# Performance work log

Measured on AMD Instinct MI355X. Metric: run time of the kernel, lower is better.

## Reference

```python
import jax, jax.numpy as jnp
import numpy as np

B, H, P, D = 32, 8, 16, 32
OUT_DIM = 32
GROUPS = 64
NUM_F = 8
N = H * P * D                 # 4096 (self.num)
PHO = P * H * OUT_DIM         # 4096


def setup_inputs() -> dict:
    key = jax.random.key(0)
    ks = jax.random.split(key, 10)
    return {
        "q": jax.random.normal(ks[0], (B, H, P, D), dtype=jnp.float32),
        "k": jax.random.normal(ks[1], (B, H, P, D), dtype=jnp.float32),
        "grid": jnp.arange(NUM_F, dtype=jnp.float32) + 1.0,
        "base_weight_q": jax.random.uniform(ks[2], (PHO, N), dtype=jnp.float32),
        "base_weight_k": jax.random.uniform(ks[3], (PHO, N), dtype=jnp.float32),
        "coef_q": jax.random.uniform(ks[4], (GROUPS, 1, NUM_F), dtype=jnp.float32),
        "coef_k": jax.random.uniform(ks[5], (GROUPS, 1, NUM_F), dtype=jnp.float32),
        # grouped 1x1 conv == num_f independent [PHO, N] matmuls (only conv_layer_q is used in forward)
        "conv_wq": jax.random.normal(ks[6], (NUM_F, PHO, N), dtype=jnp.float32) * 0.01,
        "conv_bq": jax.random.normal(ks[7], (NUM_F, PHO), dtype=jnp.float32) * 0.01,
        "scale_sp": jnp.ones((PHO,), dtype=jnp.float32),
    }


def reference(q, k, grid, base_weight_q, base_weight_k, coef_q, coef_k, conv_wq, conv_bq, scale_sp):
    b, h, p, d = q.shape
    n = h * p * d
    nf = grid.shape[0]
    gs = n // coef_q.shape[0]               # group_size
    out_dim = base_weight_q.shape[0] // (p * h)

    qf = q.reshape(b, n)
    kf = k.reshape(b, n)

    base_q = jax.nn.silu(qf) @ base_weight_q.T          # [B, PHO]
    base_k = jax.nn.silu(kf) @ base_weight_k.T

    # per-feature coef: feature i in group i//gs, scaled per frequency f -> [F, N]
    ce_q = jnp.repeat(coef_q[:, 0, :], gs, axis=0).T
    ce_k = jnp.repeat(coef_k[:, 0, :], gs, axis=0).T

    sq = jnp.sin(grid[None, :, None] * qf[:, None, :]) * ce_q[None]   # [B, F, N]
    sk = jnp.sin(grid[None, :, None] * kf[:, None, :]) * ce_k[None]

    # grouped conv1d (kernel 1, groups=num_f): per-frequency matmul; original uses conv_layer_q for both
    fq = jnp.einsum('bfn,fon->bfo', sq, conv_wq) + conv_bq[None]      # [B, F, PHO]
    fq = fq.sum(axis=1) * scale_sp
    fk = jnp.einsum('bfn,fon->bfo', sk, conv_wq) + conv_bq[None]
    fk = fk.sum(axis=1) * scale_sp

    y = (fq * scale_sp + base_q) + (fk * scale_sp + base_k)
    y = y.reshape(b, h, p, out_dim)
    return jax.nn.softmax(y, axis=-1)
```

## Files before the change

kernel.cpp:

```cpp
#include <hip/hip_runtime.h>
#include <math.h>

#define N_TOT 4096
#define PHO_T 4096
#define KTOT  40960
#define NS    2560
#define NSUP  32

typedef __attribute__((ext_vector_type(8)))  short short8v;
typedef __attribute__((ext_vector_type(16))) float f32x16;

#define GLD16(src, dst) __builtin_amdgcn_global_load_lds(                      \
    (const __attribute__((address_space(1))) void*)(src),                      \
    (__attribute__((address_space(3))) void*)(dst), 16, 0, 0)

__device__ __forceinline__ void split1(float x, short& h, short& l) {
    unsigned u  = __builtin_bit_cast(unsigned, x);
    unsigned hu = (u + 0x7FFFu + ((u >> 16) & 1u)) & 0xFFFF0000u;
    h = (short)(hu >> 16);
    float r = x - __builtin_bit_cast(float, hu);
    unsigned ur = __builtin_bit_cast(unsigned, r);
    l = (short)((ur + 0x7FFFu + ((ur >> 16) & 1u)) >> 16);
}

__global__ void act_kernel(const float* __restrict__ q,
                           const float* __restrict__ kx,
                           const float* __restrict__ grid_,
                           const float* __restrict__ coefq,
                           const float* __restrict__ coefk,
                           short* __restrict__ Af)
{
    const int t = blockIdx.x * 256 + threadIdx.x;
    const int S = t >> 6;
    const int l = t & 63;
    const int b = l & 31;
    const int k0 = S * 16 + (l >> 5) * 8;

    float v[8];
    if (k0 < 8192) {
        const float* src = (k0 < 4096) ? (q  + (size_t)b * N_TOT + k0)
                                       : (kx + (size_t)b * N_TOT + (k0 - 4096));
#pragma unroll
        for (int j = 0; j < 8; ++j) {
            const float x = src[j];
            v[j] = x / (1.f + __expf(-x));
        }
    } else {
        const int f  = (k0 - 8192) >> 12;
        const int n0 = (k0 - 8192) & 4095;
        const int g  = n0 >> 6;
        const float gf  = grid_[f];
        const float cq_ = coefq[g * 8 + f];
        const float ck_ = coefk[g * 8 + f];
        const float* qp = q  + (size_t)b * N_TOT + n0;
        const float* kp = kx + (size_t)b * N_TOT + n0;
#pragma unroll
        for (int j = 0; j < 8; ++j)
            v[j] = __sinf(gf * qp[j]) * cq_ + __sinf(gf * kp[j]) * ck_;
    }

    short8v hi, lo;
#pragma unroll
    for (int j = 0; j < 8; ++j) { short h, lw; split1(v[j], h, lw); hi[j] = h; lo[j] = lw; }
    *(short8v*)&Af[((size_t)(S * 2 + 0) * 64 + l) * 8] = hi;
    *(short8v*)&Af[((size_t)(S * 2 + 1) * 64 + l) * 8] = lo;
}

#define OBK  256
#define KC   32
#define KSUP 1280
#define NCH  (KSUP / KC)

__global__ __launch_bounds__(256) void gemm_kernel(
    const float* __restrict__ bwq, const float* __restrict__ bwk,
    const float* __restrict__ cw,  const short* __restrict__ Af,
    const float* __restrict__ ssp, float* __restrict__ ypart)
{
    __shared__ float Wl[2][OBK * KC];

    const int t  = threadIdx.x;
    const int ks = blockIdx.x >> 4;
    const int ob = blockIdx.x & 15;
    const int o_base = ob * OBK;
    const int k_base = ks * KSUP;

    const int w  = t >> 6;
    const int l  = t & 63;
    const int srow  = l >> 3;
    const int sslot = (l & 7) ^ (srow & 7);

    f32x16 accU0, accU1, accS0, accS1;
#pragma unroll
    for (int i = 0; i < 16; ++i) {
        accU0[i] = 0.f; accU1[i] = 0.f; accS0[i] = 0.f; accS1[i] = 0.f;
    }

    auto wptr = [&](int kg) -> const float* {
        if (kg < 4096)  return bwq + kg;
        if (kg < 8192)  return bwk + (kg - 4096);
        const int f    = (kg - 8192) >> 12;
        const int noff = (kg - 8192) & 4095;
        return cw + (size_t)f * (size_t)PHO_T * N_TOT + noff;
    };

    auto stage = [&](int kg, int buf) {
        const float* Wp = wptr(kg);
#pragma unroll
        for (int i = 0; i < 8; ++i) {
            const int row = w * 64 + i * 8 + srow;
            const float* src = Wp + (size_t)(o_base + row) * N_TOT + sslot * 4;
            GLD16(src, &Wl[buf][(w * 64 + i * 8) * KC]);
        }
    };

    const int rkey = l & 7;
    const int row0 = w * 64 + (l & 31);
    const int j0b  = (l >> 5) * 2;

    auto compute = [&](int kg, int cur, const short8v& ah0, const short8v& al0,
                       const short8v& ah1, const short8v& al1) {
        const bool sc = (kg >= 8192);
#pragma unroll
        for (int s = 0; s < 2; ++s) {
            const short8v& ah = s ? ah1 : ah0;
            const short8v& al = s ? al1 : al0;
            const int j0 = s * 4 + j0b;

            auto tileop = [&](int nt, f32x16& acc) {
                const float* rp = &Wl[cur][(row0 + nt * 32) * KC];
                const float4 wa = *(const float4*)&rp[((j0    ) ^ rkey) * 4];
                const float4 wb = *(const float4*)&rp[((j0 + 1) ^ rkey) * 4];
                short8v bh, bl;
                {
                    short h, lw;
                    split1(wa.x, h, lw); bh[0] = h; bl[0] = lw;
                    split1(wa.y, h, lw); bh[1] = h; bl[1] = lw;
                    split1(wa.z, h, lw); bh[2] = h; bl[2] = lw;
                    split1(wa.w, h, lw); bh[3] = h; bl[3] = lw;
                    split1(wb.x, h, lw); bh[4] = h; bl[4] = lw;
                    split1(wb.y, h, lw); bh[5] = h; bl[5] = lw;
                    split1(wb.z, h, lw); bh[6] = h; bl[6] = lw;
                    split1(wb.w, h, lw); bh[7] = h; bl[7] = lw;
                }
                acc = __builtin_amdgcn_mfma_f32_32x32x16_bf16(ah, bh, acc, 0, 0, 0);
                acc = __builtin_amdgcn_mfma_f32_32x32x16_bf16(ah, bl, acc, 0, 0, 0);
                acc = __builtin_amdgcn_mfma_f32_32x32x16_bf16(al, bh, acc, 0, 0, 0);
            };
            if (sc) { tileop(0, accS0); tileop(1, accS1); }
            else    { tileop(0, accU0); tileop(1, accU1); }
        }
    };

    stage(k_base, 0);

    short8v ah0, al0, ah1, al1;
    for (int c = 0; c < NCH - 1; ++c) {
        const int cur = c & 1;
        const int kg  = k_base + c * KC;
        const size_t Sg = (size_t)(kg >> 4);
        ah0 = *(const short8v*)&Af[(((Sg    ) * 2 + 0) * 64 + l) * 8];
        al0 = *(const short8v*)&Af[(((Sg    ) * 2 + 1) * 64 + l) * 8];
        ah1 = *(const short8v*)&Af[(((Sg + 1) * 2 + 0) * 64 + l) * 8];
        al1 = *(const short8v*)&Af[(((Sg + 1) * 2 + 1) * 64 + l) * 8];
        asm volatile("" ::: "memory");
        stage(kg + KC, cur ^ 1);
        asm volatile("s_waitcnt vmcnt(8)" ::: "memory");
        __builtin_amdgcn_sched_barrier(0);
        compute(kg, cur, ah0, al0, ah1, al1);
    }
    {
        const int c   = NCH - 1;
        const int kg  = k_base + c * KC;
        const size_t Sg = (size_t)(kg >> 4);
        ah0 = *(const short8v*)&Af[(((Sg    ) * 2 + 0) * 64 + l) * 8];
        al0 = *(const short8v*)&Af[(((Sg    ) * 2 + 1) * 64 + l) * 8];
        ah1 = *(const short8v*)&Af[(((Sg + 1) * 2 + 0) * 64 + l) * 8];
        al1 = *(const short8v*)&Af[(((Sg + 1) * 2 + 1) * 64 + l) * 8];
        asm volatile("s_waitcnt vmcnt(0)" ::: "memory");
        __builtin_amdgcn_sched_barrier(0);
        compute(kg, c & 1, ah0, al0, ah1, al1);
    }

    float* __restrict__ yp = ypart + (size_t)ks * (32 * PHO_T);
    const int o0 = o_base + w * 64 + (l & 31);
    const int o1 = o0 + 32;
    const float x0 = ssp[o0], x1 = ssp[o1];
    const float s0 = x0 * x0, s1 = x1 * x1;
    const int bh4 = 4 * (l >> 5);
#pragma unroll
    for (int r = 0; r < 16; ++r) {
        const int b = (r & 3) + 8 * (r >> 2) + bh4;
        yp[(size_t)b * PHO_T + o0] = accU0[r] + accS0[r] * s0;
        yp[(size_t)b * PHO_T + o1] = accU1[r] + accS1[r] * s1;
    }
}

__global__ void reduce_softmax_kernel(const float* __restrict__ ypart,
                                      const float* __restrict__ cb,
                                      const float* __restrict__ ssp,
                                      float* __restrict__ out)
{
    const int e = blockIdx.x * 256 + threadIdx.x;
    const int o = e & 4095;

    float v = 0.f;
#pragma unroll
    for (int ks = 0; ks < NSUP; ++ks)
        v += ypart[(size_t)ks * (32 * PHO_T) + e];

    float bias = 0.f;
#pragma unroll
    for (int f = 0; f < 8; ++f) bias += cb[f * PHO_T + o];
    const float ss = ssp[o];
    v += 2.f * ss * ss * bias;

    float m = v;
#pragma unroll
    for (int s = 16; s > 0; s >>= 1) m = fmaxf(m, __shfl_xor(m, s, 32));
    const float ex = __expf(v - m);
    float sum = ex;
#pragma unroll
    for (int s = 16; s > 0; s >>= 1) sum += __shfl_xor(sum, s, 32);
    out[e] = ex / sum;
}

extern "C" void kernel_launch(void* const* d_in, const int* in_sizes, int n_in,
                              void* d_out, int out_size, void* d_ws, size_t ws_size,
                              hipStream_t stream)
{
    const float* q    = (const float*)d_in[0];
    const float* k    = (const float*)d_in[1];
    const float* grid = (const float*)d_in[2];
    const float* bwq  = (const float*)d_in[3];
    const float* bwk  = (const float*)d_in[4];
    const float* cq   = (const float*)d_in[5];
    const float* ck   = (const float*)d_in[6];
    const float* cw   = (const float*)d_in[7];
    const float* cb   = (const float*)d_in[8];
    const float* ssp  = (const float*)d_in[9];
    float* out = (float*)d_out;

    short* Af    = (short*)d_ws;
    float* ypart = (float*)((char*)d_ws + (size_t)NS * 2 * 64 * 16);

    act_kernel<<<640, 256, 0, stream>>>(q, k, grid, cq, ck, Af);
    gemm_kernel<<<512, 256, 0, stream>>>(bwq, bwk, cw, Af, ssp, ypart);
    reduce_softmax_kernel<<<512, 256, 0, stream>>>(ypart, cb, ssp, out);
}
```

Measured before the change: 141.3 us.

## Split weight staging into halves and prefetch A fragments one chunk ahead

Weight-chunk staging and compute are split into two row halves, so the second half's global-to-LDS loads are issued while the first half is being multiplied. The A-operand fragments for the next chunk are loaded one iteration early into ping-ponged register sets, and the loop is unrolled by two to rotate them. The intent is finer-grained overlap of memory latency with MFMA work. In exchange it uses more registers, and correctness depends on hand-tuned vmcnt waits and the hard-coded trip count of 19 double-iterations plus a peeled tail.

```diff
diff --git a/kernel.cpp b/kernel.cpp
--- a/kernel.cpp
+++ b/kernel.cpp
@@ -103,83 +103,110 @@
         return cw + (size_t)f * (size_t)PHO_T * N_TOT + noff;
     };
 
-    auto stage = [&](int kg, int buf) {
+    auto stage_half = [&](int kg, int buf, int h) {
         const float* Wp = wptr(kg);
 #pragma unroll
-        for (int i = 0; i < 8; ++i) {
-            const int row = w * 64 + i * 8 + srow;
+        for (int i = 0; i < 4; ++i) {
+            const int rb  = w * 64 + h * 32 + i * 8;
+            const int row = rb + srow;
             const float* src = Wp + (size_t)(o_base + row) * N_TOT + sslot * 4;
-            GLD16(src, &Wl[buf][(w * 64 + i * 8) * KC]);
+            GLD16(src, &Wl[buf][rb * KC]);
         }
     };
 
     const int rkey = l & 7;
-    const int row0 = w * 64 + (l & 31);
     const int j0b  = (l >> 5) * 2;
 
-    auto compute = [&](int kg, int cur, const short8v& ah0, const short8v& al0,
-                       const short8v& ah1, const short8v& al1) {
+    auto compute_half = [&](int kg, int cur, int h,
+                            const short8v& ah0, const short8v& al0,
+                            const short8v& ah1, const short8v& al1,
+                            f32x16& aU, f32x16& aS) {
         const bool sc = (kg >= 8192);
+        const int rowh = w * 64 + h * 32 + (l & 31);
+        const float* rp = &Wl[cur][rowh * KC];
 #pragma unroll
         for (int s = 0; s < 2; ++s) {
             const short8v& ah = s ? ah1 : ah0;
             const short8v& al = s ? al1 : al0;
             const int j0 = s * 4 + j0b;
-
-            auto tileop = [&](int nt, f32x16& acc) {
-                const float* rp = &Wl[cur][(row0 + nt * 32) * KC];
-                const float4 wa = *(const float4*)&rp[((j0    ) ^ rkey) * 4];
-                const float4 wb = *(const float4*)&rp[((j0 + 1) ^ rkey) * 4];
-                short8v bh, bl;
-                {
-                    short h, lw;
-                    split1(wa.x, h, lw); bh[0] = h; bl[0] = lw;
-                    split1(wa.y, h, lw); bh[1] = h; bl[1] = lw;
-                    split1(wa.z, h, lw); bh[2] = h; bl[2] = lw;
-                    split1(wa.w, h, lw); bh[3] = h; bl[3] = lw;
-                    split1(wb.x, h, lw); bh[4] = h; bl[4] = lw;
-                    split1(wb.y, h, lw); bh[5] = h; bl[5] = lw;
-                    split1(wb.z, h, lw); bh[6] = h; bl[6] = lw;
-                    split1(wb.w, h, lw); bh[7] = h; bl[7] = lw;
-                }
-                acc = __builtin_amdgcn_mfma_f32_32x32x16_bf16(ah, bh, acc, 0, 0, 0);
-                acc = __builtin_amdgcn_mfma_f32_32x32x16_bf16(ah, bl, acc, 0, 0, 0);
-                acc = __builtin_amdgcn_mfma_f32_32x32x16_bf16(al, bh, acc, 0, 0, 0);
-            };
-            if (sc) { tileop(0, accS0); tileop(1, accS1); }
-            else    { tileop(0, accU0); tileop(1, accU1); }
+            const float4 wa = *(const float4*)&rp[((j0    ) ^ rkey) * 4];
+            const float4 wb = *(const float4*)&rp[((j0 + 1) ^ rkey) * 4];
+            short8v bh, bl;
+            {
+                short hh, lw;
+                split1(wa.x, hh, lw); bh[0] = hh; bl[0] = lw;
+                split1(wa.y, hh, lw); bh[1] = hh; bl[1] = lw;
+                split1(wa.z, hh, lw); bh[2] = hh; bl[2] = lw;
+                split1(wa.w, hh, lw); bh[3] = hh; bl[3] = lw;
+                split1(wb.x, hh, lw); bh[4] = hh; bl[4] = lw;
+                split1(wb.y, hh, lw); bh[5] = hh; bl[5] = lw;
+                split1(wb.z, hh, lw); bh[6] = hh; bl[6] = lw;
+                split1(wb.w, hh, lw); bh[7] = hh; bl[7] = lw;
+            }
+            f32x16& acc = sc ? aS : aU;
+            acc = __builtin_amdgcn_mfma_f32_32x32x16_bf16(ah, bh, acc, 0, 0, 0);
+            acc = __builtin_amdgcn_mfma_f32_32x32x16_bf16(ah, bl, acc, 0, 0, 0);
+            acc = __builtin_amdgcn_mfma_f32_32x32x16_bf16(al, bh, acc, 0, 0, 0);
         }
     };
 
-    stage(k_base, 0);
-
-    short8v ah0, al0, ah1, al1;
-    for (int c = 0; c < NCH - 1; ++c) {
-        const int cur = c & 1;
-        const int kg  = k_base + c * KC;
-        const size_t Sg = (size_t)(kg >> 4);
-        ah0 = *(const short8v*)&Af[(((Sg    ) * 2 + 0) * 64 + l) * 8];
-        al0 = *(const short8v*)&Af[(((Sg    ) * 2 + 1) * 64 + l) * 8];
-        ah1 = *(const short8v*)&Af[(((Sg + 1) * 2 + 0) * 64 + l) * 8];
-        al1 = *(const short8v*)&Af[(((Sg + 1) * 2 + 1) * 64 + l) * 8];
+#define LOAD_AF(Sg, H0, L0, H1, L1)                                            \
+    H0 = *(const short8v*)&Af[(((Sg)     * 2 + 0) * 64 + l) * 8];              \
+    L0 = *(const short8v*)&Af[(((Sg)     * 2 + 1) * 64 + l) * 8];              \
+    H1 = *(const short8v*)&Af[(((Sg) + 1) * 2 + 0) * 64 * 8 + l * 8];          \
+    L1 = *(const short8v*)&Af[((((Sg) + 1) * 2 + 1) * 64 + l) * 8];
+
+#undef LOAD_AF
+#define LOAD_AF(Sg, H0, L0, H1, L1)                                            \
+    H0 = *(const short8v*)&Af[(((Sg)      * 2 + 0) * 64 + l) * 8];             \
+    L0 = *(const short8v*)&Af[(((Sg)      * 2 + 1) * 64 + l) * 8];             \
+    H1 = *(const short8v*)&Af[((((Sg) + 1) * 2 + 0) * 64 + l) * 8];            \
+    L1 = *(const short8v*)&Af[((((Sg) + 1) * 2 + 1) * 64 + l) * 8];
+
+#define BODY(c, CH0, CL0, CH1, CL1, NH0, NL0, NH1, NL1) do {                   \
+    const int kg = k_base + (c) * KC;                                          \
+    const size_t Sg2 = (size_t)((kg + KC) >> 4);                               \
+    LOAD_AF(Sg2, NH0, NL0, NH1, NL1)                                           \
+    asm volatile("" ::: "memory");            \
+    stage_half(kg + KC, ((c) + 1) & 1, 0);                                     \
+    asm volatile("s_waitcnt vmcnt(12)" ::: "memory");                          \
+    __builtin_amdgcn_sched_barrier(0);                                         \
+    compute_half(kg, (c) & 1, 0, CH0, CL0, CH1, CL1, accU0, accS0);            \
+    stage_half(kg + KC, ((c) + 1) & 1, 1);                                     \
+    asm volatile("s_waitcnt vmcnt(12)" ::: "memory");                          \
+    __builtin_amdgcn_sched_barrier(0);                                         \
+    compute_half(kg, (c) & 1, 1, CH0, CL0, CH1, CL1, accU1, accS1);            \
+} while (0)
+
+    short8v a_h0, a_l0, a_h1, a_l1;
+    short8v b_h0, b_l0, b_h1, b_l1;
+
+    {
+        const size_t Sg = (size_t)(k_base >> 4);
+        LOAD_AF(Sg, a_h0, a_l0, a_h1, a_l1)
         asm volatile("" ::: "memory");
-        stage(kg + KC, cur ^ 1);
-        asm volatile("s_waitcnt vmcnt(8)" ::: "memory");
+        stage_half(k_base, 0, 0);
+        stage_half(k_base, 0, 1);
+    }
+
+    for (int cc = 0; cc < 19; ++cc) {
+        const int c = cc * 2;
+        BODY(c,     a_h0, a_l0, a_h1, a_l1,  b_h0, b_l0, b_h1, b_l1);
+        BODY(c + 1, b_h0, b_l0, b_h1, b_l1,  a_h0, a_l0, a_h1, a_l1);
+    }
+    BODY(38, a_h0, a_l0, a_h1, a_l1,  b_h0, b_l0, b_h1, b_l1);
+
+    {
+        const int kg = k_base + 39 * KC;
+        asm volatile("s_waitcnt vmcnt(4)" ::: "memory");
         __builtin_amdgcn_sched_barrier(0);
-        compute(kg, cur, ah0, al0, ah1, al1);
-    }
-    {
-        const int c   = NCH - 1;
-        const int kg  = k_base + c * KC;
-        const size_t Sg = (size_t)(kg >> 4);
-        ah0 = *(const short8v*)&Af[(((Sg    ) * 2 + 0) * 64 + l) * 8];
-        al0 = *(const short8v*)&Af[(((Sg    ) * 2 + 1) * 64 + l) * 8];
-        ah1 = *(const short8v*)&Af[(((Sg + 1) * 2 + 0) * 64 + l) * 8];
-        al1 = *(const short8v*)&Af[(((Sg + 1) * 2 + 1) * 64 + l) * 8];
+        compute_half(kg, 1, 0, b_h0, b_l0, b_h1, b_l1, accU0, accS0);
         asm volatile("s_waitcnt vmcnt(0)" ::: "memory");
         __builtin_amdgcn_sched_barrier(0);
-        compute(kg, c & 1, ah0, al0, ah1, al1);
-    }
+        compute_half(kg, 1, 1, b_h0, b_l0, b_h1, b_l1, accU1, accS1);
+    }
+#undef BODY
+#undef LOAD_AF
 
     float* __restrict__ yp = ypart + (size_t)ks * (32 * PHO_T);
     const int o0 = o_base + w * 64 + (l & 31);
```

Result: slower. 145.2 us (+2.7%).
